# Performance work log

Measured on AMD Instinct MI355X. Metric: run time of the kernel, lower is better.

## Reference

```python
import jax, jax.numpy as jnp
import numpy as np

V = 45      # vocab / input_size / output_size
H = 2048    # hidden_size
W = 128     # stack_width
D = 200     # stack_depth


def setup_inputs() -> dict:
    key = jax.random.key(0)
    ks = jax.random.split(key, 14)
    s = 0.02
    return {
        "inp": jax.random.randint(ks[0], (1,), 0, V),
        "hidden": jax.random.normal(ks[1], (1, 1, H), jnp.float32),
        "stack": jax.random.normal(ks[2], (1, D, W), jnp.float32),
        "emb": jax.random.normal(ks[3], (V, H), jnp.float32) * s,
        "ctrl_W": jax.random.normal(ks[4], (3, H), jnp.float32) * s,
        "ctrl_b": jnp.zeros((3,), jnp.float32),
        "sin_W": jax.random.normal(ks[5], (W, H), jnp.float32) * s,
        "sin_b": jnp.zeros((W,), jnp.float32),
        "w_ih": jax.random.normal(ks[6], (3 * H, H + W), jnp.float32) * s,
        "w_hh": jax.random.normal(ks[7], (3 * H, H), jnp.float32) * s,
        "b_ih": jnp.zeros((3 * H,), jnp.float32),
        "b_hh": jnp.zeros((3 * H,), jnp.float32),
        "dec_W": jax.random.normal(ks[8], (V, H), jnp.float32) * s,
        "dec_b": jnp.zeros((V,), jnp.float32),
    }


def reference(inp, hidden, stack, emb, ctrl_W, ctrl_b, sin_W, sin_b,
              w_ih, w_hh, b_ih, b_hh, dec_W, dec_b):
    h = hidden[0]  # [1, H]  (n_layers=1, unidirectional -> squeeze(0))

    # --- differentiable stack update ---
    controls = jax.nn.softmax(h @ ctrl_W.T + ctrl_b, axis=1)      # [1, 3]
    stack_input = jnp.tanh(h @ sin_W.T + sin_b)[:, None, :]       # [1, 1, W]
    zeros_bottom = jnp.zeros((1, 1, W), stack.dtype)
    stack_down = jnp.concatenate([stack[:, 1:], zeros_bottom], axis=1)   # pop
    stack_up = jnp.concatenate([stack_input, stack[:, :-1]], axis=1)    # push
    c = controls.reshape(1, 3, 1, 1)  # (push, pop, no_op)
    new_stack = c[:, 2] * stack + c[:, 0] * stack_up + c[:, 1] * stack_down
    stack_top = new_stack[:, 0, :]  # [1, W]

    # --- embed token, concat stack top ---
    x = jnp.concatenate([emb[inp].reshape(1, -1), stack_top], axis=1)  # [1, H+W]

    # --- GRU cell (PyTorch gate convention) ---
    gi = x @ w_ih.T + b_ih   # [1, 3H]
    gh = h @ w_hh.T + b_hh   # [1, 3H]
    i_r, i_z, i_n = jnp.split(gi, 3, axis=1)
    h_r, h_z, h_n = jnp.split(gh, 3, axis=1)
    r = jax.nn.sigmoid(i_r + h_r)
    z = jax.nn.sigmoid(i_z + h_z)
    n = jnp.tanh(i_n + r * h_n)
    h_new = (1.0 - z) * n + z * h   # [1, H]

    # --- decoder ---
    output = h_new @ dec_W.T + dec_b  # [1, V]
    return output, h_new[None], new_stack
```

## Files before the change

### kernel.cpp

```cpp
#include <hip/hip_runtime.h>
#include <hip/hip_bf16.h>

#define V_SZ 45
#define H_SZ 2048
#define W_SZ 128
#define D_SZ 200
#define X_SZ (H_SZ + W_SZ)

#define WS_CTRL 0
#define WS_SIN  16
#define WS_HNEW 160

__device__ __forceinline__ float dot4(float4 a, float4 b) {
  return a.x * b.x + a.y * b.y + a.z * b.z + a.w * b.w;
}

__device__ __forceinline__ float wave_reduce(float v) {
#pragma unroll
  for (int o = 32; o > 0; o >>= 1) v += __shfl_down(v, o, 64);
  return v;
}

__device__ __forceinline__ void ctrl_softmax(const float* __restrict__ ws,
                                             float& c0, float& c1, float& c2) {
  const float l0 = ws[WS_CTRL + 0], l1 = ws[WS_CTRL + 1], l2 = ws[WS_CTRL + 2];
  const float m = fmaxf(l0, fmaxf(l1, l2));
  const float e0 = __expf(l0 - m), e1 = __expf(l1 - m), e2 = __expf(l2 - m);
  const float inv = 1.f / (e0 + e1 + e2);
  c0 = e0 * inv; c1 = e1 * inv; c2 = e2 * inv;
}

__global__ __launch_bounds__(256) void k1_small_gemv(
    const float* __restrict__ hidden,
    const float* __restrict__ ctrl_W,
    const float* __restrict__ ctrl_b,
    const float* __restrict__ sin_W,
    const float* __restrict__ sin_b,
    float* __restrict__ ws) {
  const int b = blockIdx.x;
  const int tid = threadIdx.x;
  const float* row = (b < 3) ? (ctrl_W + (size_t)b * H_SZ)
                             : (sin_W + (size_t)(b - 3) * H_SZ);
  const float4* rw4 = (const float4*)row;
  const float4* rh4 = (const float4*)hidden;
  float acc = dot4(rw4[tid], rh4[tid]) + dot4(rw4[tid + 256], rh4[tid + 256]);

  acc = wave_reduce(acc);
  __shared__ float red[4];
  const int wv_id = tid >> 6;
  if ((tid & 63) == 0) red[wv_id] = acc;
  __syncthreads();
  if (tid == 0) {
    float total = red[0] + red[1] + red[2] + red[3];
    if (b < 3) {
      ws[WS_CTRL + b] = total + ctrl_b[b];
    } else {
      ws[WS_SIN + (b - 3)] = tanhf(total + sin_b[b - 3]);
    }
  }
}

__global__ __launch_bounds__(256) void k3_gru(
    const int* __restrict__ inp,
    const float* __restrict__ hidden,
    const float* __restrict__ emb,
    const float* __restrict__ stack,
    const float* __restrict__ w_ih,
    const float* __restrict__ w_hh,
    const float* __restrict__ b_ih,
    const float* __restrict__ b_hh,
    float* __restrict__ ws,
    float* __restrict__ out) {
  const int tid = threadIdx.x;
  const int j = blockIdx.x;

  float a0 = 0.f, a1 = 0.f, a2 = 0.f, a3 = 0.f, a4 = 0.f, a5 = 0.f;

  const float4* wi0 = (const float4*)(w_ih + (size_t)j * X_SZ);
  const float4* wi1 = (const float4*)(w_ih + (size_t)(j + H_SZ) * X_SZ);
  const float4* wi2 = (const float4*)(w_ih + (size_t)(j + 2 * H_SZ) * X_SZ);
  const float4* emb4 = (const float4*)(emb + (size_t)inp[0] * H_SZ);

#pragma unroll
  for (int q = 0; q < 2; ++q) {
    const int c = tid + q * 256;
    const float4 xv = emb4[c];
    a0 += dot4(wi0[c], xv);
    a1 += dot4(wi1[c], xv);
    a2 += dot4(wi2[c], xv);
  }
  if (tid < (X_SZ - H_SZ) / 4) {
    const int c = 512 + tid;
    const int w = 4 * tid;
    float c0, c1, c2;
    ctrl_softmax(ws, c0, c1, c2);
    const float4 s0 = *(const float4*)(stack + w);
    const float4 s1 = *(const float4*)(stack + W_SZ + w);
    const float4 sv = *(const float4*)(ws + WS_SIN + w);
    float4 xv;
    xv.x = c2 * s0.x + c0 * sv.x + c1 * s1.x;
    xv.y = c2 * s0.y + c0 * sv.y + c1 * s1.y;
    xv.z = c2 * s0.z + c0 * sv.z + c1 * s1.z;
    xv.w = c2 * s0.w + c0 * sv.w + c1 * s1.w;
    a0 += dot4(wi0[c], xv);
    a1 += dot4(wi1[c], xv);
    a2 += dot4(wi2[c], xv);
  }

  const float4* wh0 = (const float4*)(w_hh + (size_t)j * H_SZ);
  const float4* wh1 = (const float4*)(w_hh + (size_t)(j + H_SZ) * H_SZ);
  const float4* wh2 = (const float4*)(w_hh + (size_t)(j + 2 * H_SZ) * H_SZ);
  const float4* h4 = (const float4*)hidden;
#pragma unroll
  for (int q = 0; q < 2; ++q) {
    const int c = tid + q * 256;
    const float4 hv = h4[c];
    a3 += dot4(wh0[c], hv);
    a4 += dot4(wh1[c], hv);
    a5 += dot4(wh2[c], hv);
  }

  a0 = wave_reduce(a0); a1 = wave_reduce(a1); a2 = wave_reduce(a2);
  a3 = wave_reduce(a3); a4 = wave_reduce(a4); a5 = wave_reduce(a5);
  __shared__ float red[4][6];
  const int wv_id = tid >> 6;
  if ((tid & 63) == 0) {
    red[wv_id][0] = a0; red[wv_id][1] = a1; red[wv_id][2] = a2;
    red[wv_id][3] = a3; red[wv_id][4] = a4; red[wv_id][5] = a5;
  }
  __syncthreads();
  if (tid == 0) {
    float t[6];
#pragma unroll
    for (int q = 0; q < 6; ++q)
      t[q] = red[0][q] + red[1][q] + red[2][q] + red[3][q];
    const float gi_r = t[0] + b_ih[j];
    const float gi_z = t[1] + b_ih[j + H_SZ];
    const float gi_n = t[2] + b_ih[j + 2 * H_SZ];
    const float gh_r = t[3] + b_hh[j];
    const float gh_z = t[4] + b_hh[j + H_SZ];
    const float gh_n = t[5] + b_hh[j + 2 * H_SZ];
    const float r = 1.f / (1.f + __expf(-(gi_r + gh_r)));
    const float z = 1.f / (1.f + __expf(-(gi_z + gh_z)));
    const float n = tanhf(gi_n + r * gh_n);
    const float hn = (1.f - z) * n + z * hidden[j];
    ws[WS_HNEW + j] = hn;
    out[V_SZ + j] = hn;
  }
}

__global__ __launch_bounds__(256) void k4_dec_stack(
    const float* __restrict__ dec_W,
    const float* __restrict__ dec_b,
    const float* __restrict__ stack,
    float* __restrict__ ws,
    float* __restrict__ out) {
  const int tid = threadIdx.x;
  if (blockIdx.x < V_SZ) {
    const int v = blockIdx.x;
    const float4* row = (const float4*)(dec_W + (size_t)v * H_SZ);
    const float4* h4 = (const float4*)(ws + WS_HNEW);
    float acc = dot4(row[tid], h4[tid]) + dot4(row[tid + 256], h4[tid + 256]);
    acc = wave_reduce(acc);
    __shared__ float red[4];
    const int wv_id = tid >> 6;
    if ((tid & 63) == 0) red[wv_id] = acc;
    __syncthreads();
    if (tid == 0) out[v] = red[0] + red[1] + red[2] + red[3] + dec_b[v];
  } else {
    const int i = (blockIdx.x - V_SZ) * 256 + tid;
    float c0, c1, c2;
    ctrl_softmax(ws, c0, c1, c2);
    const int d = i >> 7;
    const int w = i & (W_SZ - 1);
    const float s = stack[i];
    const float up = (d == 0) ? ws[WS_SIN + w] : stack[i - W_SZ];
    const float dn = (d == D_SZ - 1) ? 0.f : stack[i + W_SZ];
    out[V_SZ + H_SZ + i] = c2 * s + c0 * up + c1 * dn;
  }
}

extern "C" void kernel_launch(void* const* d_in, const int* in_sizes, int n_in,
                              void* d_out, int out_size, void* d_ws, size_t ws_size,
                              hipStream_t stream) {
  const int*   inp    = (const int*)d_in[0];
  const float* hidden = (const float*)d_in[1];
  const float* stack  = (const float*)d_in[2];
  const float* emb    = (const float*)d_in[3];
  const float* ctrl_W = (const float*)d_in[4];
  const float* ctrl_b = (const float*)d_in[5];
  const float* sin_W  = (const float*)d_in[6];
  const float* sin_b  = (const float*)d_in[7];
  const float* w_ih   = (const float*)d_in[8];
  const float* w_hh   = (const float*)d_in[9];
  const float* b_ih   = (const float*)d_in[10];
  const float* b_hh   = (const float*)d_in[11];
  const float* dec_W  = (const float*)d_in[12];
  const float* dec_b  = (const float*)d_in[13];
  float* out = (float*)d_out;
  float* ws = (float*)d_ws;

  k1_small_gemv<<<3 + W_SZ, 256, 0, stream>>>(hidden, ctrl_W, ctrl_b, sin_W, sin_b, ws);
  k3_gru<<<H_SZ, 256, 0, stream>>>(inp, hidden, emb, stack, w_ih, w_hh, b_ih, b_hh, ws, out);
  k4_dec_stack<<<V_SZ + (D_SZ * W_SZ) / 256, 256, 0, stream>>>(dec_W, dec_b, stack, ws, out);
}
```

Baseline: 153.5 us.

## Fuse all stages into one cooperative kernel with grid syncs

Replaces the three launches with one cooperative kernel of 1024 blocks, each computing two GRU hidden units, with grid-wide syncs between stages. Most of the w_ih and w_hh dot products are issued before the first sync, so the weight streaming overlaps the small controller and stack-input GEMV instead of waiting behind it. This removes kernel launch gaps and inter-kernel drains. In exchange it adds two grid barriers and depends on the cooperative launch succeeding; if it fails, the old three-kernel path runs.

New measurement: 397.6 us. +159.0%, slower.

```diff
diff --git a/kernel.cpp b/kernel.cpp
--- a/kernel.cpp
+++ b/kernel.cpp
@@ -1,5 +1,7 @@
 #include <hip/hip_runtime.h>
-#include <hip/hip_bf16.h>
+#include <hip/hip_cooperative_groups.h>
+
+namespace cg = cooperative_groups;
 
 #define V_SZ 45
 #define H_SZ 2048
@@ -30,13 +32,176 @@
   c0 = e0 * inv; c1 = e1 * inv; c2 = e2 * inv;
 }
 
-__global__ __launch_bounds__(256) void k1_small_gemv(
+__global__ __launch_bounds__(256, 4) void fused_all(
+    const int* __restrict__ inp,
     const float* __restrict__ hidden,
+    const float* __restrict__ stack,
+    const float* __restrict__ emb,
     const float* __restrict__ ctrl_W,
     const float* __restrict__ ctrl_b,
     const float* __restrict__ sin_W,
     const float* __restrict__ sin_b,
-    float* __restrict__ ws) {
+    const float* __restrict__ w_ih,
+    const float* __restrict__ w_hh,
+    const float* __restrict__ b_ih,
+    const float* __restrict__ b_hh,
+    const float* __restrict__ dec_W,
+    const float* __restrict__ dec_b,
+    float* __restrict__ ws,
+    float* __restrict__ out) {
+  cg::grid_group grid = cg::this_grid();
+  const int tid = threadIdx.x;
+  const int b = blockIdx.x;
+  const size_t j0 = (size_t)(2 * b);
+  const size_t j1 = j0 + 1;
+
+  __shared__ float smem[4][12];
+  __shared__ float sred[4];
+
+  const float4* wi0 = (const float4*)(w_ih + j0 * X_SZ);
+  const float4* wi1 = (const float4*)(w_ih + (j0 + H_SZ) * X_SZ);
+  const float4* wi2 = (const float4*)(w_ih + (j0 + 2 * H_SZ) * X_SZ);
+  const float4* wi3 = (const float4*)(w_ih + j1 * X_SZ);
+  const float4* wi4 = (const float4*)(w_ih + (j1 + H_SZ) * X_SZ);
+  const float4* wi5 = (const float4*)(w_ih + (j1 + 2 * H_SZ) * X_SZ);
+  const float4* wh0 = (const float4*)(w_hh + j0 * H_SZ);
+  const float4* wh1 = (const float4*)(w_hh + (j0 + H_SZ) * H_SZ);
+  const float4* wh2 = (const float4*)(w_hh + (j0 + 2 * H_SZ) * H_SZ);
+  const float4* wh3 = (const float4*)(w_hh + j1 * H_SZ);
+  const float4* wh4 = (const float4*)(w_hh + (j1 + H_SZ) * H_SZ);
+  const float4* wh5 = (const float4*)(w_hh + (j1 + 2 * H_SZ) * H_SZ);
+  const float4* emb4 = (const float4*)(emb + (size_t)inp[0] * H_SZ);
+  const float4* h4 = (const float4*)hidden;
+
+  float ai0 = 0.f, ai1 = 0.f, ai2 = 0.f, ai3 = 0.f, ai4 = 0.f, ai5 = 0.f;
+  float ah0 = 0.f, ah1 = 0.f, ah2 = 0.f, ah3 = 0.f, ah4 = 0.f, ah5 = 0.f;
+
+#pragma unroll
+  for (int q = 0; q < 2; ++q) {
+    const int c = tid + q * 256;
+    const float4 xv = emb4[c];
+    ai0 += dot4(wi0[c], xv);
+    ai1 += dot4(wi1[c], xv);
+    ai2 += dot4(wi2[c], xv);
+    ai3 += dot4(wi3[c], xv);
+    ai4 += dot4(wi4[c], xv);
+    ai5 += dot4(wi5[c], xv);
+  }
+#pragma unroll
+  for (int q = 0; q < 2; ++q) {
+    const int c = tid + q * 256;
+    const float4 hv = h4[c];
+    ah0 += dot4(wh0[c], hv);
+    ah1 += dot4(wh1[c], hv);
+    ah2 += dot4(wh2[c], hv);
+    ah3 += dot4(wh3[c], hv);
+    ah4 += dot4(wh4[c], hv);
+    ah5 += dot4(wh5[c], hv);
+  }
+
+  if (b < 3 + W_SZ) {
+    const float* row = (b < 3) ? (ctrl_W + (size_t)b * H_SZ)
+                               : (sin_W + (size_t)(b - 3) * H_SZ);
+    const float4* r4 = (const float4*)row;
+    float acc = dot4(r4[tid], h4[tid]) + dot4(r4[tid + 256], h4[tid + 256]);
+    acc = wave_reduce(acc);
+    if ((tid & 63) == 0) sred[tid >> 6] = acc;
+    __syncthreads();
+    if (tid == 0) {
+      const float total = sred[0] + sred[1] + sred[2] + sred[3];
+      if (b < 3) ws[WS_CTRL + b] = total + ctrl_b[b];
+      else       ws[WS_SIN + (b - 3)] = tanhf(total + sin_b[b - 3]);
+    }
+  }
+
+  grid.sync();
+
+  if (tid < 32) {
+    float c0, c1, c2;
+    ctrl_softmax(ws, c0, c1, c2);
+    const int c = 512 + tid;
+    const int w = 4 * tid;
+    const float4 s0 = *(const float4*)(stack + w);
+    const float4 s1 = *(const float4*)(stack + W_SZ + w);
+    const float4 sv = *(const float4*)(ws + WS_SIN + w);
+    float4 xv;
+    xv.x = c2 * s0.x + c0 * sv.x + c1 * s1.x;
+    xv.y = c2 * s0.y + c0 * sv.y + c1 * s1.y;
+    xv.z = c2 * s0.z + c0 * sv.z + c1 * s1.z;
+    xv.w = c2 * s0.w + c0 * sv.w + c1 * s1.w;
+    ai0 += dot4(wi0[c], xv);
+    ai1 += dot4(wi1[c], xv);
+    ai2 += dot4(wi2[c], xv);
+    ai3 += dot4(wi3[c], xv);
+    ai4 += dot4(wi4[c], xv);
+    ai5 += dot4(wi5[c], xv);
+  }
+
+  ai0 = wave_reduce(ai0); ai1 = wave_reduce(ai1); ai2 = wave_reduce(ai2);
+  ai3 = wave_reduce(ai3); ai4 = wave_reduce(ai4); ai5 = wave_reduce(ai5);
+  ah0 = wave_reduce(ah0); ah1 = wave_reduce(ah1); ah2 = wave_reduce(ah2);
+  ah3 = wave_reduce(ah3); ah4 = wave_reduce(ah4); ah5 = wave_reduce(ah5);
+  {
+    const int wv = tid >> 6;
+    if ((tid & 63) == 0) {
+      smem[wv][0] = ai0; smem[wv][1] = ai1; smem[wv][2] = ai2;
+      smem[wv][3] = ah0; smem[wv][4] = ah1; smem[wv][5] = ah2;
+      smem[wv][6] = ai3; smem[wv][7] = ai4; smem[wv][8] = ai5;
+      smem[wv][9] = ah3; smem[wv][10] = ah4; smem[wv][11] = ah5;
+    }
+  }
+  __syncthreads();
+  if (tid < 2) {
+    const int p = tid;
+    const size_t j = j0 + p;
+    float t[6];
+#pragma unroll
+    for (int k = 0; k < 6; ++k)
+      t[k] = smem[0][p * 6 + k] + smem[1][p * 6 + k] +
+             smem[2][p * 6 + k] + smem[3][p * 6 + k];
+    const float gi_r = t[0] + b_ih[j];
+    const float gi_z = t[1] + b_ih[j + H_SZ];
+    const float gi_n = t[2] + b_ih[j + 2 * H_SZ];
+    const float gh_r = t[3] + b_hh[j];
+    const float gh_z = t[4] + b_hh[j + H_SZ];
+    const float gh_n = t[5] + b_hh[j + 2 * H_SZ];
+    const float r = 1.f / (1.f + __expf(-(gi_r + gh_r)));
+    const float z = 1.f / (1.f + __expf(-(gi_z + gh_z)));
+    const float n = tanhf(gi_n + r * gh_n);
+    const float hn = (1.f - z) * n + z * hidden[j];
+    ws[WS_HNEW + j] = hn;
+    out[V_SZ + j] = hn;
+  }
+
+  grid.sync();
+
+  if (b < V_SZ) {
+    const float4* row = (const float4*)(dec_W + (size_t)b * H_SZ);
+    const float4* hn4 = (const float4*)(ws + WS_HNEW);
+    float acc = dot4(row[tid], hn4[tid]) + dot4(row[tid + 256], hn4[tid + 256]);
+    acc = wave_reduce(acc);
+    __syncthreads();
+    if ((tid & 63) == 0) sred[tid >> 6] = acc;
+    __syncthreads();
+    if (tid == 0)
+      out[b] = sred[0] + sred[1] + sred[2] + sred[3] + dec_b[b];
+  } else if (b < V_SZ + (D_SZ * W_SZ) / 256) {
+    const int i = (b - V_SZ) * 256 + tid;
+    float c0, c1, c2;
+    ctrl_softmax(ws, c0, c1, c2);
+    const int d = i >> 7;
+    const int w = i & (W_SZ - 1);
+    const float s = stack[i];
+    const float up = (d == 0) ? ws[WS_SIN + w] : stack[i - W_SZ];
+    const float dn = (d == D_SZ - 1) ? 0.f : stack[i + W_SZ];
+    out[V_SZ + H_SZ + i] = c2 * s + c0 * up + c1 * dn;
+  }
+}
+
+__global__ __launch_bounds__(256) void k1_small_gemv(
+    const float* __restrict__ hidden, const float* __restrict__ ctrl_W,
+    const float* __restrict__ ctrl_b, const float* __restrict__ sin_W,
+    const float* __restrict__ sin_b, float* __restrict__ ws) {
   const int b = blockIdx.x;
   const int tid = threadIdx.x;
   const float* row = (b < 3) ? (ctrl_W + (size_t)b * H_SZ)
@@ -44,50 +209,35 @@
   const float4* rw4 = (const float4*)row;
   const float4* rh4 = (const float4*)hidden;
   float acc = dot4(rw4[tid], rh4[tid]) + dot4(rw4[tid + 256], rh4[tid + 256]);
-
   acc = wave_reduce(acc);
   __shared__ float red[4];
-  const int wv_id = tid >> 6;
-  if ((tid & 63) == 0) red[wv_id] = acc;
+  if ((tid & 63) == 0) red[tid >> 6] = acc;
   __syncthreads();
   if (tid == 0) {
     float total = red[0] + red[1] + red[2] + red[3];
-    if (b < 3) {
-      ws[WS_CTRL + b] = total + ctrl_b[b];
-    } else {
-      ws[WS_SIN + (b - 3)] = tanhf(total + sin_b[b - 3]);
-    }
+    if (b < 3) ws[WS_CTRL + b] = total + ctrl_b[b];
+    else       ws[WS_SIN + (b - 3)] = tanhf(total + sin_b[b - 3]);
   }
 }
 
 __global__ __launch_bounds__(256) void k3_gru(
-    const int* __restrict__ inp,
-    const float* __restrict__ hidden,
-    const float* __restrict__ emb,
-    const float* __restrict__ stack,
-    const float* __restrict__ w_ih,
-    const float* __restrict__ w_hh,
-    const float* __restrict__ b_ih,
-    const float* __restrict__ b_hh,
-    float* __restrict__ ws,
-    float* __restrict__ out) {
+    const int* __restrict__ inp, const float* __restrict__ hidden,
+    const float* __restrict__ emb, const float* __restrict__ stack,
+    const float* __restrict__ w_ih, const float* __restrict__ w_hh,
+    const float* __restrict__ b_ih, const float* __restrict__ b_hh,
+    float* __restrict__ ws, float* __restrict__ out) {
   const int tid = threadIdx.x;
   const int j = blockIdx.x;
-
   float a0 = 0.f, a1 = 0.f, a2 = 0.f, a3 = 0.f, a4 = 0.f, a5 = 0.f;
-
   const float4* wi0 = (const float4*)(w_ih + (size_t)j * X_SZ);
   const float4* wi1 = (const float4*)(w_ih + (size_t)(j + H_SZ) * X_SZ);
   const float4* wi2 = (const float4*)(w_ih + (size_t)(j + 2 * H_SZ) * X_SZ);
   const float4* emb4 = (const float4*)(emb + (size_t)inp[0] * H_SZ);
-
 #pragma unroll
   for (int q = 0; q < 2; ++q) {
     const int c = tid + q * 256;
     const float4 xv = emb4[c];
-    a0 += dot4(wi0[c], xv);
-    a1 += dot4(wi1[c], xv);
-    a2 += dot4(wi2[c], xv);
+    a0 += dot4(wi0[c], xv); a1 += dot4(wi1[c], xv); a2 += dot4(wi2[c], xv);
   }
   if (tid < (X_SZ - H_SZ) / 4) {
     const int c = 512 + tid;
@@ -102,11 +252,8 @@
     xv.y = c2 * s0.y + c0 * sv.y + c1 * s1.y;
     xv.z = c2 * s0.z + c0 * sv.z + c1 * s1.z;
     xv.w = c2 * s0.w + c0 * sv.w + c1 * s1.w;
-    a0 += dot4(wi0[c], xv);
-    a1 += dot4(wi1[c], xv);
-    a2 += dot4(wi2[c], xv);
-  }
-
+    a0 += dot4(wi0[c], xv); a1 += dot4(wi1[c], xv); a2 += dot4(wi2[c], xv);
+  }
   const float4* wh0 = (const float4*)(w_hh + (size_t)j * H_SZ);
   const float4* wh1 = (const float4*)(w_hh + (size_t)(j + H_SZ) * H_SZ);
   const float4* wh2 = (const float4*)(w_hh + (size_t)(j + 2 * H_SZ) * H_SZ);
@@ -115,18 +262,15 @@
   for (int q = 0; q < 2; ++q) {
     const int c = tid + q * 256;
     const float4 hv = h4[c];
-    a3 += dot4(wh0[c], hv);
-    a4 += dot4(wh1[c], hv);
-    a5 += dot4(wh2[c], hv);
-  }
-
+    a3 += dot4(wh0[c], hv); a4 += dot4(wh1[c], hv); a5 += dot4(wh2[c], hv);
+  }
   a0 = wave_reduce(a0); a1 = wave_reduce(a1); a2 = wave_reduce(a2);
   a3 = wave_reduce(a3); a4 = wave_reduce(a4); a5 = wave_reduce(a5);
   __shared__ float red[4][6];
-  const int wv_id = tid >> 6;
+  const int wv = tid >> 6;
   if ((tid & 63) == 0) {
-    red[wv_id][0] = a0; red[wv_id][1] = a1; red[wv_id][2] = a2;
-    red[wv_id][3] = a3; red[wv_id][4] = a4; red[wv_id][5] = a5;
+    red[wv][0] = a0; red[wv][1] = a1; red[wv][2] = a2;
+    red[wv][3] = a3; red[wv][4] = a4; red[wv][5] = a5;
   }
   __syncthreads();
   if (tid == 0) {
@@ -150,21 +294,18 @@
 }
 
 __global__ __launch_bounds__(256) void k4_dec_stack(
-    const float* __restrict__ dec_W,
-    const float* __restrict__ dec_b,
-    const float* __restrict__ stack,
-    float* __restrict__ ws,
+    const float* __restrict__ dec_W, const float* __restrict__ dec_b,
+    const float* __restrict__ stack, float* __restrict__ ws,
     float* __restrict__ out) {
   const int tid = threadIdx.x;
   if (blockIdx.x < V_SZ) {
     const int v = blockIdx.x;
     const float4* row = (const float4*)(dec_W + (size_t)v * H_SZ);
-    const float4* h4 = (const float4*)(ws + WS_HNEW);
-    float acc = dot4(row[tid], h4[tid]) + dot4(row[tid + 256], h4[tid + 256]);
+    const float4* hn4 = (const float4*)(ws + WS_HNEW);
+    float acc = dot4(row[tid], hn4[tid]) + dot4(row[tid + 256], hn4[tid + 256]);
     acc = wave_reduce(acc);
     __shared__ float red[4];
-    const int wv_id = tid >> 6;
-    if ((tid & 63) == 0) red[wv_id] = acc;
+    if ((tid & 63) == 0) red[tid >> 6] = acc;
     __syncthreads();
     if (tid == 0) out[v] = red[0] + red[1] + red[2] + red[3] + dec_b[v];
   } else {
@@ -200,7 +341,16 @@
   float* out = (float*)d_out;
   float* ws = (float*)d_ws;
 
-  k1_small_gemv<<<3 + W_SZ, 256, 0, stream>>>(hidden, ctrl_W, ctrl_b, sin_W, sin_b, ws);
-  k3_gru<<<H_SZ, 256, 0, stream>>>(inp, hidden, emb, stack, w_ih, w_hh, b_ih, b_hh, ws, out);
-  k4_dec_stack<<<V_SZ + (D_SZ * W_SZ) / 256, 256, 0, stream>>>(dec_W, dec_b, stack, ws, out);
-}
+  void* args[] = {(void*)&inp, (void*)&hidden, (void*)&stack, (void*)&emb,
+                  (void*)&ctrl_W, (void*)&ctrl_b, (void*)&sin_W, (void*)&sin_b,
+                  (void*)&w_ih, (void*)&w_hh, (void*)&b_ih, (void*)&b_hh,
+                  (void*)&dec_W, (void*)&dec_b, (void*)&ws, (void*)&out};
+  hipError_t err = hipLaunchCooperativeKernel((const void*)fused_all,
+                                              dim3(1024), dim3(256),
+                                              args, 0, stream);
+  if (err != hipSuccess) {
+    k1_small_gemv<<<3 + W_SZ, 256, 0, stream>>>(hidden, ctrl_W, ctrl_b, sin_W, sin_b, ws);
+    k3_gru<<<H_SZ, 256, 0, stream>>>(inp, hidden, emb, stack, w_ih, w_hh, b_ih, b_hh, ws, out);
+    k4_dec_stack<<<V_SZ + (D_SZ * W_SZ) / 256, 256, 0, stream>>>(dec_W, dec_b, stack, ws, out);
+  }
+}
```

## Fuse stack-control GEMV into GRU kernel with atomic flag handoff

Applied to the files above, without the earlier changes.

Merges the small ctrl/sin GEMV kernel into the GRU kernel. The first 131 blocks compute those rows and signal completion through a global atomic counter, and every block spin-waits on that counter only before it needs the stack-top input. Each block now handles two hidden units, giving 1024 blocks, and the w_hh and embedding partial dots are computed before the wait so they overlap. This removes one kernel launch and its serialization, but adds a memset launch and spin-wait synchronisation. That wait relies on the producer blocks being scheduled, which is assumed safe here because they have the lowest block indices.

Result: slower. 167.1 us (+8.8%).

```diff
diff --git a/kernel.cpp b/kernel.cpp
--- a/kernel.cpp
+++ b/kernel.cpp
@@ -1,5 +1,4 @@
 #include <hip/hip_runtime.h>
-#include <hip/hip_bf16.h>
 
 #define V_SZ 45
 #define H_SZ 2048
@@ -10,6 +9,7 @@
 #define WS_CTRL 0
 #define WS_SIN  16
 #define WS_HNEW 160
+#define WS_FLAG 2304
 
 __device__ __forceinline__ float dot4(float4 a, float4 b) {
   return a.x * b.x + a.y * b.y + a.z * b.z + a.w * b.w;
@@ -30,41 +30,15 @@
   c0 = e0 * inv; c1 = e1 * inv; c2 = e2 * inv;
 }
 
-__global__ __launch_bounds__(256) void k1_small_gemv(
+__global__ __launch_bounds__(256, 4) void fused_gru(
+    const int* __restrict__ inp,
     const float* __restrict__ hidden,
+    const float* __restrict__ stack,
+    const float* __restrict__ emb,
     const float* __restrict__ ctrl_W,
     const float* __restrict__ ctrl_b,
     const float* __restrict__ sin_W,
     const float* __restrict__ sin_b,
-    float* __restrict__ ws) {
-  const int b = blockIdx.x;
-  const int tid = threadIdx.x;
-  const float* row = (b < 3) ? (ctrl_W + (size_t)b * H_SZ)
-                             : (sin_W + (size_t)(b - 3) * H_SZ);
-  const float4* rw4 = (const float4*)row;
-  const float4* rh4 = (const float4*)hidden;
-  float acc = dot4(rw4[tid], rh4[tid]) + dot4(rw4[tid + 256], rh4[tid + 256]);
-
-  acc = wave_reduce(acc);
-  __shared__ float red[4];
-  const int wv_id = tid >> 6;
-  if ((tid & 63) == 0) red[wv_id] = acc;
-  __syncthreads();
-  if (tid == 0) {
-    float total = red[0] + red[1] + red[2] + red[3];
-    if (b < 3) {
-      ws[WS_CTRL + b] = total + ctrl_b[b];
-    } else {
-      ws[WS_SIN + (b - 3)] = tanhf(total + sin_b[b - 3]);
-    }
-  }
-}
-
-__global__ __launch_bounds__(256) void k3_gru(
-    const int* __restrict__ inp,
-    const float* __restrict__ hidden,
-    const float* __restrict__ emb,
-    const float* __restrict__ stack,
     const float* __restrict__ w_ih,
     const float* __restrict__ w_hh,
     const float* __restrict__ b_ih,
@@ -72,28 +46,86 @@
     float* __restrict__ ws,
     float* __restrict__ out) {
   const int tid = threadIdx.x;
-  const int j = blockIdx.x;
-
-  float a0 = 0.f, a1 = 0.f, a2 = 0.f, a3 = 0.f, a4 = 0.f, a5 = 0.f;
-
-  const float4* wi0 = (const float4*)(w_ih + (size_t)j * X_SZ);
-  const float4* wi1 = (const float4*)(w_ih + (size_t)(j + H_SZ) * X_SZ);
-  const float4* wi2 = (const float4*)(w_ih + (size_t)(j + 2 * H_SZ) * X_SZ);
+  const int b = blockIdx.x;
+  const size_t j0 = (size_t)(2 * b);
+  const size_t j1 = j0 + 1;
+  int* flag = (int*)(ws + WS_FLAG);
+
+  __shared__ float smem[4][12];
+  __shared__ float sred[4];
+
+  const float4* h4 = (const float4*)hidden;
+
+  if (b < 3 + W_SZ) {
+    const float* row = (b < 3) ? (ctrl_W + (size_t)b * H_SZ)
+                               : (sin_W + (size_t)(b - 3) * H_SZ);
+    const float4* r4 = (const float4*)row;
+    float acc = dot4(r4[tid], h4[tid]) + dot4(r4[tid + 256], h4[tid + 256]);
+    acc = wave_reduce(acc);
+    if ((tid & 63) == 0) sred[tid >> 6] = acc;
+    __syncthreads();
+    if (tid == 0) {
+      const float total = sred[0] + sred[1] + sred[2] + sred[3];
+      if (b < 3) ws[WS_CTRL + b] = total + ctrl_b[b];
+      else       ws[WS_SIN + (b - 3)] = tanhf(total + sin_b[b - 3]);
+      __hip_atomic_fetch_add(flag, 1, __ATOMIC_RELEASE,
+                             __HIP_MEMORY_SCOPE_AGENT);
+    }
+  }
+
+  const float4* wi0 = (const float4*)(w_ih + j0 * X_SZ);
+  const float4* wi1 = (const float4*)(w_ih + (j0 + H_SZ) * X_SZ);
+  const float4* wi2 = (const float4*)(w_ih + (j0 + 2 * H_SZ) * X_SZ);
+  const float4* wi3 = (const float4*)(w_ih + j1 * X_SZ);
+  const float4* wi4 = (const float4*)(w_ih + (j1 + H_SZ) * X_SZ);
+  const float4* wi5 = (const float4*)(w_ih + (j1 + 2 * H_SZ) * X_SZ);
+  const float4* wh0 = (const float4*)(w_hh + j0 * H_SZ);
+  const float4* wh1 = (const float4*)(w_hh + (j0 + H_SZ) * H_SZ);
+  const float4* wh2 = (const float4*)(w_hh + (j0 + 2 * H_SZ) * H_SZ);
+  const float4* wh3 = (const float4*)(w_hh + j1 * H_SZ);
+  const float4* wh4 = (const float4*)(w_hh + (j1 + H_SZ) * H_SZ);
+  const float4* wh5 = (const float4*)(w_hh + (j1 + 2 * H_SZ) * H_SZ);
   const float4* emb4 = (const float4*)(emb + (size_t)inp[0] * H_SZ);
+
+  float ai0 = 0.f, ai1 = 0.f, ai2 = 0.f, ai3 = 0.f, ai4 = 0.f, ai5 = 0.f;
+  float ah0 = 0.f, ah1 = 0.f, ah2 = 0.f, ah3 = 0.f, ah4 = 0.f, ah5 = 0.f;
 
 #pragma unroll
   for (int q = 0; q < 2; ++q) {
     const int c = tid + q * 256;
     const float4 xv = emb4[c];
-    a0 += dot4(wi0[c], xv);
-    a1 += dot4(wi1[c], xv);
-    a2 += dot4(wi2[c], xv);
-  }
-  if (tid < (X_SZ - H_SZ) / 4) {
+    ai0 += dot4(wi0[c], xv);
+    ai1 += dot4(wi1[c], xv);
+    ai2 += dot4(wi2[c], xv);
+    ai3 += dot4(wi3[c], xv);
+    ai4 += dot4(wi4[c], xv);
+    ai5 += dot4(wi5[c], xv);
+  }
+#pragma unroll
+  for (int q = 0; q < 2; ++q) {
+    const int c = tid + q * 256;
+    const float4 hv = h4[c];
+    ah0 += dot4(wh0[c], hv);
+    ah1 += dot4(wh1[c], hv);
+    ah2 += dot4(wh2[c], hv);
+    ah3 += dot4(wh3[c], hv);
+    ah4 += dot4(wh4[c], hv);
+    ah5 += dot4(wh5[c], hv);
+  }
+
+  if (tid == 0) {
+    while (__hip_atomic_load(flag, __ATOMIC_ACQUIRE,
+                             __HIP_MEMORY_SCOPE_AGENT) < 3 + W_SZ) {
+      __builtin_amdgcn_s_sleep(2);
+    }
+  }
+  __syncthreads();
+
+  if (tid < 32) {
+    float c0, c1, c2;
+    ctrl_softmax(ws, c0, c1, c2);
     const int c = 512 + tid;
     const int w = 4 * tid;
-    float c0, c1, c2;
-    ctrl_softmax(ws, c0, c1, c2);
     const float4 s0 = *(const float4*)(stack + w);
     const float4 s1 = *(const float4*)(stack + W_SZ + w);
     const float4 sv = *(const float4*)(ws + WS_SIN + w);
@@ -102,38 +134,36 @@
     xv.y = c2 * s0.y + c0 * sv.y + c1 * s1.y;
     xv.z = c2 * s0.z + c0 * sv.z + c1 * s1.z;
     xv.w = c2 * s0.w + c0 * sv.w + c1 * s1.w;
-    a0 += dot4(wi0[c], xv);
-    a1 += dot4(wi1[c], xv);
-    a2 += dot4(wi2[c], xv);
-  }
-
-  const float4* wh0 = (const float4*)(w_hh + (size_t)j * H_SZ);
-  const float4* wh1 = (const float4*)(w_hh + (size_t)(j + H_SZ) * H_SZ);
-  const float4* wh2 = (const float4*)(w_hh + (size_t)(j + 2 * H_SZ) * H_SZ);
-  const float4* h4 = (const float4*)hidden;
-#pragma unroll
-  for (int q = 0; q < 2; ++q) {
-    const int c = tid + q * 256;
-    const float4 hv = h4[c];
-    a3 += dot4(wh0[c], hv);
-    a4 += dot4(wh1[c], hv);
-    a5 += dot4(wh2[c], hv);
-  }
-
-  a0 = wave_reduce(a0); a1 = wave_reduce(a1); a2 = wave_reduce(a2);
-  a3 = wave_reduce(a3); a4 = wave_reduce(a4); a5 = wave_reduce(a5);
-  __shared__ float red[4][6];
-  const int wv_id = tid >> 6;
-  if ((tid & 63) == 0) {
-    red[wv_id][0] = a0; red[wv_id][1] = a1; red[wv_id][2] = a2;
-    red[wv_id][3] = a3; red[wv_id][4] = a4; red[wv_id][5] = a5;
+    ai0 += dot4(wi0[c], xv);
+    ai1 += dot4(wi1[c], xv);
+    ai2 += dot4(wi2[c], xv);
+    ai3 += dot4(wi3[c], xv);
+    ai4 += dot4(wi4[c], xv);
+    ai5 += dot4(wi5[c], xv);
+  }
+
+  ai0 = wave_reduce(ai0); ai1 = wave_reduce(ai1); ai2 = wave_reduce(ai2);
+  ai3 = wave_reduce(ai3); ai4 = wave_reduce(ai4); ai5 = wave_reduce(ai5);
+  ah0 = wave_reduce(ah0); ah1 = wave_reduce(ah1); ah2 = wave_reduce(ah2);
+  ah3 = wave_reduce(ah3); ah4 = wave_reduce(ah4); ah5 = wave_reduce(ah5);
+  {
+    const int wv = tid >> 6;
+    if ((tid & 63) == 0) {
+      smem[wv][0] = ai0; smem[wv][1] = ai1; smem[wv][2] = ai2;
+      smem[wv][3] = ah0; smem[wv][4] = ah1; smem[wv][5] = ah2;
+      smem[wv][6] = ai3; smem[wv][7] = ai4; smem[wv][8] = ai5;
+      smem[wv][9] = ah3; smem[wv][10] = ah4; smem[wv][11] = ah5;
+    }
   }
   __syncthreads();
-  if (tid == 0) {
+  if (tid < 2) {
+    const int p = tid;
+    const size_t j = j0 + p;
     float t[6];
 #pragma unroll
-    for (int q = 0; q < 6; ++q)
-      t[q] = red[0][q] + red[1][q] + red[2][q] + red[3][q];
+    for (int k = 0; k < 6; ++k)
+      t[k] = smem[0][p * 6 + k] + smem[1][p * 6 + k] +
+             smem[2][p * 6 + k] + smem[3][p * 6 + k];
     const float gi_r = t[0] + b_ih[j];
     const float gi_z = t[1] + b_ih[j + H_SZ];
     const float gi_n = t[2] + b_ih[j + 2 * H_SZ];
@@ -150,21 +180,18 @@
 }
 
 __global__ __launch_bounds__(256) void k4_dec_stack(
-    const float* __restrict__ dec_W,
-    const float* __restrict__ dec_b,
-    const float* __restrict__ stack,
-    float* __restrict__ ws,
+    const float* __restrict__ dec_W, const float* __restrict__ dec_b,
+    const float* __restrict__ stack, float* __restrict__ ws,
     float* __restrict__ out) {
   const int tid = threadIdx.x;
   if (blockIdx.x < V_SZ) {
     const int v = blockIdx.x;
     const float4* row = (const float4*)(dec_W + (size_t)v * H_SZ);
-    const float4* h4 = (const float4*)(ws + WS_HNEW);
-    float acc = dot4(row[tid], h4[tid]) + dot4(row[tid + 256], h4[tid + 256]);
+    const float4* hn4 = (const float4*)(ws + WS_HNEW);
+    float acc = dot4(row[tid], hn4[tid]) + dot4(row[tid + 256], hn4[tid + 256]);
     acc = wave_reduce(acc);
     __shared__ float red[4];
-    const int wv_id = tid >> 6;
-    if ((tid & 63) == 0) red[wv_id] = acc;
+    if ((tid & 63) == 0) red[tid >> 6] = acc;
     __syncthreads();
     if (tid == 0) out[v] = red[0] + red[1] + red[2] + red[3] + dec_b[v];
   } else {
@@ -200,7 +227,11 @@
   float* out = (float*)d_out;
   float* ws = (float*)d_ws;
 
-  k1_small_gemv<<<3 + W_SZ, 256, 0, stream>>>(hidden, ctrl_W, ctrl_b, sin_W, sin_b, ws);
-  k3_gru<<<H_SZ, 256, 0, stream>>>(inp, hidden, emb, stack, w_ih, w_hh, b_ih, b_hh, ws, out);
-  k4_dec_stack<<<V_SZ + (D_SZ * W_SZ) / 256, 256, 0, stream>>>(dec_W, dec_b, stack, ws, out);
-}
+  hipMemsetAsync((char*)d_ws + WS_FLAG * sizeof(float), 0, sizeof(int), stream);
+
+  fused_gru<<<1024, 256, 0, stream>>>(inp, hidden, stack, emb, ctrl_W, ctrl_b,
+                                      sin_W, sin_b, w_ih, w_hh, b_ih, b_hh,
+                                      ws, out);
+  k4_dec_stack<<<V_SZ + (D_SZ * W_SZ) / 256, 256, 0, stream>>>(dec_W, dec_b,
+                                                               stack, ws, out);
+}
```

## Split GRU into independent row-dot kernel plus stack-dependent gate kernel

Applied to the files above, without the earlier changes.

Restructures the pipeline so the first kernel computes every large row dot product in one launch (w_ih embedding part, w_hh, ctrl_W, sin_W), four rows per block, with no dependence on the stack update. A second small kernel adds the stack-top contribution of w_ih, computed from the softmax controls and tanh stack input, then applies the GRU gates. This takes the small control GEMV off the critical path before the large weight stream and spreads more blocks across the GPU. In exchange, partial sums make an extra round trip through workspace, the control and stack-input activation work is repeated in later kernels, and each w_ih row is now read in two separate pieces.

After: 155.9 us. No clear change (+1.6%).

```diff
diff --git a/kernel.cpp b/kernel.cpp
--- a/kernel.cpp
+++ b/kernel.cpp
@@ -1,15 +1,18 @@
 #include <hip/hip_runtime.h>
-#include <hip/hip_bf16.h>
 
 #define V_SZ 45
 #define H_SZ 2048
 #define W_SZ 128
 #define D_SZ 200
 #define X_SZ (H_SZ + W_SZ)
-
-#define WS_CTRL 0
-#define WS_SIN  16
-#define WS_HNEW 160
+#define N_IH 6144
+#define N_HH 6144
+#define N_TASKS 12419
+
+#define WS_PART     0
+#define WS_CTRL_RAW 12288
+#define WS_SIN_RAW  12291
+#define WS_HNEW     12420
 
 __device__ __forceinline__ float dot4(float4 a, float4 b) {
   return a.x * b.x + a.y * b.y + a.z * b.z + a.w * b.w;
@@ -21,125 +24,122 @@
   return v;
 }
 
-__device__ __forceinline__ void ctrl_softmax(const float* __restrict__ ws,
-                                             float& c0, float& c1, float& c2) {
-  const float l0 = ws[WS_CTRL + 0], l1 = ws[WS_CTRL + 1], l2 = ws[WS_CTRL + 2];
+__global__ __launch_bounds__(256) void kA_rowdots(
+    const int* __restrict__ inp,
+    const float* __restrict__ hidden,
+    const float* __restrict__ emb,
+    const float* __restrict__ w_ih,
+    const float* __restrict__ w_hh,
+    const float* __restrict__ ctrl_W,
+    const float* __restrict__ sin_W,
+    float* __restrict__ ws) {
+  const int tid = threadIdx.x;
+  const int b = blockIdx.x;
+  const int t0 = 4 * b;
+
+  const float4* v4 = (b < 1536) ? (const float4*)(emb + (size_t)inp[0] * H_SZ)
+                                : (const float4*)hidden;
+  const float4 va = v4[tid];
+  const float4 vb = v4[tid + 256];
+
+  const float* p0;
+  const float* p1;
+  const float* p2;
+  const float* p3;
+  {
+    const int t = t0;
+    auto rowp = [&](int tt) -> const float* {
+      if (tt < N_IH)        return w_ih + (size_t)tt * X_SZ;
+      if (tt < 12288)       return w_hh + (size_t)(tt - N_IH) * H_SZ;
+      if (tt < 12291)       return ctrl_W + (size_t)(tt - 12288) * H_SZ;
+      if (tt < N_TASKS)     return sin_W + (size_t)(tt - 12291) * H_SZ;
+      return w_hh;
+    };
+    p0 = rowp(t);
+    p1 = rowp(t + 1);
+    p2 = rowp(t + 2);
+    p3 = rowp(t + 3);
+  }
+
+  const float4* r0 = (const float4*)p0;
+  const float4* r1 = (const float4*)p1;
+  const float4* r2 = (const float4*)p2;
+  const float4* r3 = (const float4*)p3;
+
+  const float4 w0a = r0[tid], w0b = r0[tid + 256];
+  const float4 w1a = r1[tid], w1b = r1[tid + 256];
+  const float4 w2a = r2[tid], w2b = r2[tid + 256];
+  const float4 w3a = r3[tid], w3b = r3[tid + 256];
+
+  float a0 = dot4(w0a, va) + dot4(w0b, vb);
+  float a1 = dot4(w1a, va) + dot4(w1b, vb);
+  float a2 = dot4(w2a, va) + dot4(w2b, vb);
+  float a3 = dot4(w3a, va) + dot4(w3b, vb);
+
+  a0 = wave_reduce(a0);
+  a1 = wave_reduce(a1);
+  a2 = wave_reduce(a2);
+  a3 = wave_reduce(a3);
+
+  __shared__ float red[4][4];
+  const int wv = tid >> 6;
+  if ((tid & 63) == 0) {
+    red[wv][0] = a0; red[wv][1] = a1; red[wv][2] = a2; red[wv][3] = a3;
+  }
+  __syncthreads();
+  if (tid < 4 && t0 + tid < N_TASKS) {
+    ws[WS_PART + t0 + tid] =
+        red[0][tid] + red[1][tid] + red[2][tid] + red[3][tid];
+  }
+}
+
+__global__ __launch_bounds__(256) void kB_gates(
+    const float* __restrict__ stack,
+    const float* __restrict__ ctrl_b,
+    const float* __restrict__ sin_b,
+    const float* __restrict__ w_ih,
+    const float* __restrict__ b_ih,
+    const float* __restrict__ b_hh,
+    const float* __restrict__ hidden,
+    float* __restrict__ ws,
+    float* __restrict__ out) {
+  const int lane = threadIdx.x & 63;
+  const int j = (blockIdx.x * 256 + threadIdx.x) >> 6;
+
+  const float l0 = ws[WS_CTRL_RAW + 0] + ctrl_b[0];
+  const float l1 = ws[WS_CTRL_RAW + 1] + ctrl_b[1];
+  const float l2 = ws[WS_CTRL_RAW + 2] + ctrl_b[2];
   const float m = fmaxf(l0, fmaxf(l1, l2));
   const float e0 = __expf(l0 - m), e1 = __expf(l1 - m), e2 = __expf(l2 - m);
   const float inv = 1.f / (e0 + e1 + e2);
-  c0 = e0 * inv; c1 = e1 * inv; c2 = e2 * inv;
-}
-
-__global__ __launch_bounds__(256) void k1_small_gemv(
-    const float* __restrict__ hidden,
-    const float* __restrict__ ctrl_W,
-    const float* __restrict__ ctrl_b,
-    const float* __restrict__ sin_W,
-    const float* __restrict__ sin_b,
-    float* __restrict__ ws) {
-  const int b = blockIdx.x;
-  const int tid = threadIdx.x;
-  const float* row = (b < 3) ? (ctrl_W + (size_t)b * H_SZ)
-                             : (sin_W + (size_t)(b - 3) * H_SZ);
-  const float4* rw4 = (const float4*)row;
-  const float4* rh4 = (const float4*)hidden;
-  float acc = dot4(rw4[tid], rh4[tid]) + dot4(rw4[tid + 256], rh4[tid + 256]);
-
-  acc = wave_reduce(acc);
-  __shared__ float red[4];
-  const int wv_id = tid >> 6;
-  if ((tid & 63) == 0) red[wv_id] = acc;
-  __syncthreads();
-  if (tid == 0) {
-    float total = red[0] + red[1] + red[2] + red[3];
-    if (b < 3) {
-      ws[WS_CTRL + b] = total + ctrl_b[b];
-    } else {
-      ws[WS_SIN + (b - 3)] = tanhf(total + sin_b[b - 3]);
-    }
-  }
-}
-
-__global__ __launch_bounds__(256) void k3_gru(
-    const int* __restrict__ inp,
-    const float* __restrict__ hidden,
-    const float* __restrict__ emb,
-    const float* __restrict__ stack,
-    const float* __restrict__ w_ih,
-    const float* __restrict__ w_hh,
-    const float* __restrict__ b_ih,
-    const float* __restrict__ b_hh,
-    float* __restrict__ ws,
-    float* __restrict__ out) {
-  const int tid = threadIdx.x;
-  const int j = blockIdx.x;
-
-  float a0 = 0.f, a1 = 0.f, a2 = 0.f, a3 = 0.f, a4 = 0.f, a5 = 0.f;
-
-  const float4* wi0 = (const float4*)(w_ih + (size_t)j * X_SZ);
-  const float4* wi1 = (const float4*)(w_ih + (size_t)(j + H_SZ) * X_SZ);
-  const float4* wi2 = (const float4*)(w_ih + (size_t)(j + 2 * H_SZ) * X_SZ);
-  const float4* emb4 = (const float4*)(emb + (size_t)inp[0] * H_SZ);
-
-#pragma unroll
-  for (int q = 0; q < 2; ++q) {
-    const int c = tid + q * 256;
-    const float4 xv = emb4[c];
-    a0 += dot4(wi0[c], xv);
-    a1 += dot4(wi1[c], xv);
-    a2 += dot4(wi2[c], xv);
-  }
-  if (tid < (X_SZ - H_SZ) / 4) {
-    const int c = 512 + tid;
-    const int w = 4 * tid;
-    float c0, c1, c2;
-    ctrl_softmax(ws, c0, c1, c2);
-    const float4 s0 = *(const float4*)(stack + w);
-    const float4 s1 = *(const float4*)(stack + W_SZ + w);
-    const float4 sv = *(const float4*)(ws + WS_SIN + w);
-    float4 xv;
-    xv.x = c2 * s0.x + c0 * sv.x + c1 * s1.x;
-    xv.y = c2 * s0.y + c0 * sv.y + c1 * s1.y;
-    xv.z = c2 * s0.z + c0 * sv.z + c1 * s1.z;
-    xv.w = c2 * s0.w + c0 * sv.w + c1 * s1.w;
-    a0 += dot4(wi0[c], xv);
-    a1 += dot4(wi1[c], xv);
-    a2 += dot4(wi2[c], xv);
-  }
-
-  const float4* wh0 = (const float4*)(w_hh + (size_t)j * H_SZ);
-  const float4* wh1 = (const float4*)(w_hh + (size_t)(j + H_SZ) * H_SZ);
-  const float4* wh2 = (const float4*)(w_hh + (size_t)(j + 2 * H_SZ) * H_SZ);
-  const float4* h4 = (const float4*)hidden;
-#pragma unroll
-  for (int q = 0; q < 2; ++q) {
-    const int c = tid + q * 256;
-    const float4 hv = h4[c];
-    a3 += dot4(wh0[c], hv);
-    a4 += dot4(wh1[c], hv);
-    a5 += dot4(wh2[c], hv);
-  }
-
-  a0 = wave_reduce(a0); a1 = wave_reduce(a1); a2 = wave_reduce(a2);
-  a3 = wave_reduce(a3); a4 = wave_reduce(a4); a5 = wave_reduce(a5);
-  __shared__ float red[4][6];
-  const int wv_id = tid >> 6;
-  if ((tid & 63) == 0) {
-    red[wv_id][0] = a0; red[wv_id][1] = a1; red[wv_id][2] = a2;
-    red[wv_id][3] = a3; red[wv_id][4] = a4; red[wv_id][5] = a5;
-  }
-  __syncthreads();
-  if (tid == 0) {
-    float t[6];
-#pragma unroll
-    for (int q = 0; q < 6; ++q)
-      t[q] = red[0][q] + red[1][q] + red[2][q] + red[3][q];
-    const float gi_r = t[0] + b_ih[j];
-    const float gi_z = t[1] + b_ih[j + H_SZ];
-    const float gi_n = t[2] + b_ih[j + 2 * H_SZ];
-    const float gh_r = t[3] + b_hh[j];
-    const float gh_z = t[4] + b_hh[j + H_SZ];
-    const float gh_n = t[5] + b_hh[j + 2 * H_SZ];
+  const float c0 = e0 * inv, c1 = e1 * inv, c2 = e2 * inv;
+
+  const int q0 = 2 * lane, q1 = q0 + 1;
+  const float sv0 = tanhf(ws[WS_SIN_RAW + q0] + sin_b[q0]);
+  const float sv1 = tanhf(ws[WS_SIN_RAW + q1] + sin_b[q1]);
+  const float st0 = c2 * stack[q0] + c0 * sv0 + c1 * stack[W_SZ + q0];
+  const float st1 = c2 * stack[q1] + c0 * sv1 + c1 * stack[W_SZ + q1];
+
+  const float* tr = w_ih + (size_t)j * X_SZ + H_SZ;
+  const float* tz = w_ih + (size_t)(j + 2048) * X_SZ + H_SZ;
+  const float* tn = w_ih + (size_t)(j + 4096) * X_SZ + H_SZ;
+  const float2 wr = *(const float2*)(tr + q0);
+  const float2 wz = *(const float2*)(tz + q0);
+  const float2 wn = *(const float2*)(tn + q0);
+  float dr = wr.x * st0 + wr.y * st1;
+  float dz = wz.x * st0 + wz.y * st1;
+  float dn = wn.x * st0 + wn.y * st1;
+  dr = wave_reduce(dr);
+  dz = wave_reduce(dz);
+  dn = wave_reduce(dn);
+
+  if (lane == 0) {
+    const float gi_r = ws[WS_PART + j]        + dr + b_ih[j];
+    const float gi_z = ws[WS_PART + 2048 + j] + dz + b_ih[j + 2048];
+    const float gi_n = ws[WS_PART + 4096 + j] + dn + b_ih[j + 4096];
+    const float gh_r = ws[WS_PART + N_IH + j]        + b_hh[j];
+    const float gh_z = ws[WS_PART + N_IH + 2048 + j] + b_hh[j + 2048];
+    const float gh_n = ws[WS_PART + N_IH + 4096 + j] + b_hh[j + 4096];
     const float r = 1.f / (1.f + __expf(-(gi_r + gh_r)));
     const float z = 1.f / (1.f + __expf(-(gi_z + gh_z)));
     const float n = tanhf(gi_n + r * gh_n);
@@ -149,32 +149,39 @@
   }
 }
 
-__global__ __launch_bounds__(256) void k4_dec_stack(
+__global__ __launch_bounds__(256) void kC_dec_stack(
     const float* __restrict__ dec_W,
     const float* __restrict__ dec_b,
     const float* __restrict__ stack,
+    const float* __restrict__ ctrl_b,
+    const float* __restrict__ sin_b,
     float* __restrict__ ws,
     float* __restrict__ out) {
   const int tid = threadIdx.x;
   if (blockIdx.x < V_SZ) {
     const int v = blockIdx.x;
     const float4* row = (const float4*)(dec_W + (size_t)v * H_SZ);
-    const float4* h4 = (const float4*)(ws + WS_HNEW);
-    float acc = dot4(row[tid], h4[tid]) + dot4(row[tid + 256], h4[tid + 256]);
+    const float4* hn4 = (const float4*)(ws + WS_HNEW);
+    float acc = dot4(row[tid], hn4[tid]) + dot4(row[tid + 256], hn4[tid + 256]);
     acc = wave_reduce(acc);
     __shared__ float red[4];
-    const int wv_id = tid >> 6;
-    if ((tid & 63) == 0) red[wv_id] = acc;
+    if ((tid & 63) == 0) red[tid >> 6] = acc;
     __syncthreads();
     if (tid == 0) out[v] = red[0] + red[1] + red[2] + red[3] + dec_b[v];
   } else {
     const int i = (blockIdx.x - V_SZ) * 256 + tid;
-    float c0, c1, c2;
-    ctrl_softmax(ws, c0, c1, c2);
+    const float l0 = ws[WS_CTRL_RAW + 0] + ctrl_b[0];
+    const float l1 = ws[WS_CTRL_RAW + 1] + ctrl_b[1];
+    const float l2 = ws[WS_CTRL_RAW + 2] + ctrl_b[2];
+    const float m = fmaxf(l0, fmaxf(l1, l2));
+    const float e0 = __expf(l0 - m), e1 = __expf(l1 - m), e2 = __expf(l2 - m);
+    const float inv = 1.f / (e0 + e1 + e2);
+    const float c0 = e0 * inv, c1 = e1 * inv, c2 = e2 * inv;
     const int d = i >> 7;
     const int w = i & (W_SZ - 1);
     const float s = stack[i];
-    const float up = (d == 0) ? ws[WS_SIN + w] : stack[i - W_SZ];
+    const float up = (d == 0) ? tanhf(ws[WS_SIN_RAW + w] + sin_b[w])
+                              : stack[i - W_SZ];
     const float dn = (d == D_SZ - 1) ? 0.f : stack[i + W_SZ];
     out[V_SZ + H_SZ + i] = c2 * s + c0 * up + c1 * dn;
   }
@@ -200,7 +207,10 @@
   float* out = (float*)d_out;
   float* ws = (float*)d_ws;
 
-  k1_small_gemv<<<3 + W_SZ, 256, 0, stream>>>(hidden, ctrl_W, ctrl_b, sin_W, sin_b, ws);
-  k3_gru<<<H_SZ, 256, 0, stream>>>(inp, hidden, emb, stack, w_ih, w_hh, b_ih, b_hh, ws, out);
-  k4_dec_stack<<<V_SZ + (D_SZ * W_SZ) / 256, 256, 0, stream>>>(dec_W, dec_b, stack, ws, out);
-}
+  kA_rowdots<<<(N_TASKS + 3) / 4, 256, 0, stream>>>(
+      inp, hidden, emb, w_ih, w_hh, ctrl_W, sin_W, ws);
+  kB_gates<<<512, 256, 0, stream>>>(
+      stack, ctrl_b, sin_b, w_ih, b_ih, b_hh, hidden, ws, out);
+  kC_dec_stack<<<V_SZ + (D_SZ * W_SZ) / 256, 256, 0, stream>>>(
+      dec_W, dec_b, stack, ctrl_b, sin_b, ws, out);
+}
```
